# Kernel optimization log

Hardware: AMD Instinct MI355X
Metric: run time of the kernel (lower is better)

Reference implementation:

```python
import jax, jax.numpy as jnp
import numpy as np

N = 50000      # nodes
E = 800000     # edges (avg degree 16)
F_IN = 256
HID = 256
N_CLASSES = 128


def setup_inputs() -> dict:
    key = jax.random.key(0)
    ks = jax.random.split(key, 12)
    x = jax.random.normal(ks[0], (N, F_IN), dtype=jnp.float32)
    src = jax.random.randint(ks[1], (E,), 0, N)
    dst = jax.random.randint(ks[2], (E,), 0, N)
    inp = {"x": x, "src": src, "dst": dst}
    dims = [(F_IN, HID), (HID, HID), (HID, N_CLASSES)]
    for l, (din, dout) in enumerate(dims):
        s = 1.0 / np.sqrt(din)
        inp[f"W_self_{l}"] = jax.random.uniform(ks[3 + 3 * l], (dout, din), jnp.float32, -s, s)
        inp[f"W_neigh_{l}"] = jax.random.uniform(ks[4 + 3 * l], (dout, din), jnp.float32, -s, s)
        inp[f"b_{l}"] = jnp.zeros((dout,), jnp.float32)
    return inp


def _mean_agg(h, src, dst, n):
    # mean over in-neighbors: gather src features, segment-sum into dst, divide by in-degree
    s = jax.ops.segment_sum(h[src], dst, num_segments=n)          # [N, F]
    deg = jax.ops.segment_sum(jnp.ones((src.shape[0],), h.dtype), dst, num_segments=n)
    return s / jnp.maximum(deg, 1.0)[:, None]


def reference(x, W_self_0, W_neigh_0, b_0, W_self_1, W_neigh_1, b_1,
              W_self_2, W_neigh_2, b_2, src, dst):
    # DGL SAGEConv('mean'): out = fc_self(h_dst) + fc_neigh(mean_neigh(h)) + bias
    layers = [(W_self_0, W_neigh_0, b_0),
              (W_self_1, W_neigh_1, b_1),
              (W_self_2, W_neigh_2, b_2)]
    n = x.shape[0]
    h = x
    for l, (Ws, Wn, b) in enumerate(layers):
        agg = _mean_agg(h, src, dst, n)
        h = h @ Ws.T + agg @ Wn.T + b
        if l != len(layers) - 1:
            h = jax.nn.relu(h)  # dropout p=0 -> identity
    return h
```

## Files before the change

### kernel.cpp

```cpp
#include <hip/hip_runtime.h>
#include <stdint.h>

#define NNODES 50000
#define NEDGES 800000
#define NB_SCAN ((NNODES + 255) / 256)
#define NB_CVTX 12500
#define NB_CVTW 384
#define NB_HIST 3125

typedef _Float16 f16;
typedef _Float16 f16x4 __attribute__((ext_vector_type(4)));
typedef _Float16 f16x8 __attribute__((ext_vector_type(8)));
typedef float f32x4 __attribute__((ext_vector_type(4)));
typedef float f32x8 __attribute__((ext_vector_type(8)));

static inline size_t align_up(size_t x, size_t a){ return (x + a - 1) & ~(a - 1); }

__device__ __forceinline__ void gll16(const void* g, void* l){
  __builtin_amdgcn_global_load_lds((const __attribute__((address_space(1))) uint32_t*)(g),
                                   (__attribute__((address_space(3))) uint32_t*)(l), 16, 0, 0);
}

__device__ __forceinline__ f16x8 ld8(const f16* p){ return *reinterpret_cast<const f16x8*>(p); }

__global__ void __launch_bounds__(256) k_pre(const float* __restrict__ x, f16* __restrict__ xh,
                       const float* __restrict__ a0, const float* __restrict__ a1,
                       const float* __restrict__ a2, const float* __restrict__ a3,
                       const float* __restrict__ a4, const float* __restrict__ a5,
                       f16* __restrict__ o0, f16* __restrict__ o1, f16* __restrict__ o2,
                       f16* __restrict__ o3, f16* __restrict__ o4, f16* __restrict__ o5,
                       const int* __restrict__ dst, int* __restrict__ deg){
  int b = blockIdx.x;
  int tid = threadIdx.x;
  if (b < NB_CVTX){
    int i = b * 256 + tid;
    float4 v = *reinterpret_cast<const float4*>(&x[(size_t)i * 4]);
    f16x4 o = { (f16)v.x, (f16)v.y, (f16)v.z, (f16)v.w };
    *reinterpret_cast<f16x4*>(&xh[(size_t)i * 4]) = o;
  } else if (b < NB_CVTX + NB_CVTW){
    int bb = b - NB_CVTX;
    int seg = bb >> 6;
    const float* in; f16* out; int n;
    switch (seg){
      case 0: in = a0; out = o0; n = 65536; break;
      case 1: in = a1; out = o1; n = 65536; break;
      case 2: in = a2; out = o2; n = 65536; break;
      case 3: in = a3; out = o3; n = 65536; break;
      case 4: in = a4; out = o4; n = 32768; break;
      default: in = a5; out = o5; n = 32768; break;
    }
    int i = ((bb & 63) * 256 + tid) * 4;
    if (i < n){
      float4 v = *reinterpret_cast<const float4*>(&in[i]);
      f16x4 o = { (f16)v.x, (f16)v.y, (f16)v.z, (f16)v.w };
      *reinterpret_cast<f16x4*>(&out[i]) = o;
    }
  } else {
    int i = (b - NB_CVTX - NB_CVTW) * 256 + tid;
    if (i < NEDGES) atomicAdd(&deg[dst[i]], 1);
  }
}

__global__ void __launch_bounds__(256) k_scan1(const int* __restrict__ deg,
                        int* __restrict__ row_ptr, int* __restrict__ bsum, int n){
  __shared__ int s[256];
  int tid = threadIdx.x;
  int i = blockIdx.x * 256 + tid;
  int v = (i < n) ? deg[i] : 0;
  s[tid] = v;
  __syncthreads();
  #pragma unroll
  for (int off = 1; off < 256; off <<= 1){
    int t = (tid >= off) ? s[tid - off] : 0;
    __syncthreads();
    s[tid] += t;
    __syncthreads();
  }
  if (i < n) row_ptr[i] = s[tid] - v;
  if (tid == 255) bsum[blockIdx.x] = s[255];
}

__global__ void __launch_bounds__(256) k_scan2(const int* __restrict__ bsum,
                        int* __restrict__ boff, int* __restrict__ row_ptr, int nb, int n){
  __shared__ int s[256];
  int tid = threadIdx.x;
  int v = (tid < nb) ? bsum[tid] : 0;
  s[tid] = v;
  __syncthreads();
  #pragma unroll
  for (int off = 1; off < 256; off <<= 1){
    int t = (tid >= off) ? s[tid - off] : 0;
    __syncthreads();
    s[tid] += t;
    __syncthreads();
  }
  if (tid < nb) boff[tid] = s[tid] - v;
  if (tid == 255) row_ptr[n] = s[255];
}

__global__ void __launch_bounds__(256) k_scan3(int* __restrict__ row_ptr,
                        const int* __restrict__ boff, int* __restrict__ cursor, int n){
  int i = blockIdx.x * 256 + threadIdx.x;
  if (i < n){
    int v = row_ptr[i] + boff[blockIdx.x];
    row_ptr[i] = v;
    cursor[i] = v;
  }
}

__global__ void k_fill(const int* __restrict__ src, const int* __restrict__ dst,
                       int* __restrict__ cursor, int* __restrict__ csr, int e){
  int i = blockIdx.x * blockDim.x + threadIdx.x;
  if (i < e){
    int p = atomicAdd(&cursor[dst[i]], 1);
    csr[p] = src[i];
  }
}

__global__ void __launch_bounds__(256) k_mm(const f16* __restrict__ A,
                                            const f16* __restrict__ Bw,
                                            f16* __restrict__ C, int M, int N){
  __shared__ __align__(16) char sA[16384];
  __shared__ __align__(16) char sB[16384];
  int nwg = gridDim.x;
  int q = nwg >> 3, r = nwg & 7;
  int xcd = blockIdx.x & 7, seq = blockIdx.x >> 3;
  int t = (xcd < r) ? xcd * (q + 1) + seq : r * (q + 1) + (xcd - r) * q + seq;
  int nbn = N >> 7;
  int mi = t / nbn, ni = t - mi * nbn;
  int m0 = mi * 128, n0 = ni * 128;

  int tid = threadIdx.x;
  int lane = tid & 63, wid = tid >> 6;
  int wm = (wid & 1) * 64, wn = (wid >> 1) * 64;

  f32x4 acc[4][4];
  #pragma unroll
  for (int m = 0; m < 4; ++m)
    #pragma unroll
    for (int n = 0; n < 4; ++n)
      acc[m][n] = (f32x4){0.f, 0.f, 0.f, 0.f};

  const int srow = tid >> 3;
  const int scolx = ((tid & 7) << 4) ^ ((srow & 7) << 4);
  const char* Ab = (const char*)A;
  const char* Bb = (const char*)Bw;

  for (int kt = 0; kt < 4; ++kt){
    int kbyte = kt * 128;
    if (kt) __syncthreads();
    #pragma unroll
    for (int qq = 0; qq < 4; ++qq){
      int row = qq * 32 + srow;
      int ga = m0 + row; if (ga >= M) ga = M - 1;
      int gb = n0 + row;
      gll16(Ab + (size_t)ga * 512 + kbyte + scolx, sA + qq * 4096 + wid * 1024);
      gll16(Bb + (size_t)gb * 512 + kbyte + scolx, sB + qq * 4096 + wid * 1024);
    }
    __syncthreads();
    #pragma unroll
    for (int kk = 0; kk < 2; ++kk){
      int cb = kk * 64 + ((lane >> 4) << 4);
      f16x8 af[4], bfr[4];
      #pragma unroll
      for (int m = 0; m < 4; ++m){
        int rr = wm + m * 16 + (lane & 15);
        af[m] = *reinterpret_cast<const f16x8*>(sA + rr * 128 + (cb ^ ((rr & 7) << 4)));
      }
      #pragma unroll
      for (int n = 0; n < 4; ++n){
        int rr = wn + n * 16 + (lane & 15);
        bfr[n] = *reinterpret_cast<const f16x8*>(sB + rr * 128 + (cb ^ ((rr & 7) << 4)));
      }
      #pragma unroll
      for (int m = 0; m < 4; ++m)
        #pragma unroll
        for (int n = 0; n < 4; ++n)
          acc[m][n] = __builtin_amdgcn_mfma_f32_16x16x32_f16(af[m], bfr[n], acc[m][n], 0, 0, 0);
    }
  }

  int cl = lane & 15, rq = lane >> 4;
  #pragma unroll
  for (int n = 0; n < 4; ++n){
    int gc = n0 + wn + n * 16 + cl;
    #pragma unroll
    for (int m = 0; m < 4; ++m){
      int gr0 = m0 + wm + m * 16 + rq * 4;
      #pragma unroll
      for (int j = 0; j < 4; ++j){
        int gr = gr0 + j;
        if (gr < M) C[(size_t)gr * N + gc] = (f16)acc[m][n][j];
      }
    }
  }
}

__global__ void __launch_bounds__(256) k_comb(const f16* __restrict__ sp,
                        const int* __restrict__ row_ptr,
                        const int* __restrict__ csr,
                        const float* __restrict__ bias,
                        f16* __restrict__ h){
  int wid = threadIdx.x >> 6, lane = threadIdx.x & 63;
  int node = blockIdx.x * 4 + wid;
  if (node >= NNODES) return;
  int s = row_ptr[node], e = row_ptr[node + 1];
  int hh = lane >> 5, fl = lane & 31;
  const f16* pbase = sp + 256 + (size_t)fl * 8;
  f32x8 accA = {0,0,0,0,0,0,0,0}, accB = {0,0,0,0,0,0,0,0};
  int p = s + hh;
  while (p + 2 < e){
    int j0 = csr[p], j1 = csr[p + 2];
    f16x8 v0 = ld8(pbase + (size_t)j0 * 512);
    f16x8 v1 = ld8(pbase + (size_t)j1 * 512);
    #pragma unroll
    for (int c = 0; c < 8; ++c){ accA[c] += (float)v0[c]; accB[c] += (float)v1[c]; }
    p += 4;
  }
  if (p < e){
    int j = csr[p];
    f16x8 v = ld8(pbase + (size_t)j * 512);
    #pragma unroll
    for (int c = 0; c < 8; ++c) accA[c] += (float)v[c];
  }
  #pragma unroll
  for (int c = 0; c < 8; ++c){
    float t = accA[c] + accB[c];
    accA[c] = t + __shfl_xor(t, 32);
  }
  int d = e - s;
  float inv = (d > 0) ? 1.f / (float)d : 0.f;
  if (lane < 32){
    f16x8 sv = ld8(&sp[(size_t)node * 512 + fl * 8]);
    float4 ba = *reinterpret_cast<const float4*>(&bias[fl * 8]);
    float4 bb = *reinterpret_cast<const float4*>(&bias[fl * 8 + 4]);
    float bv[8] = {ba.x, ba.y, ba.z, ba.w, bb.x, bb.y, bb.z, bb.w};
    f16x8 o;
    #pragma unroll
    for (int c = 0; c < 8; ++c){
      float x = (float)sv[c] + bv[c] + accA[c] * inv;
      o[c] = (f16)fmaxf(x, 0.f);
    }
    *reinterpret_cast<f16x8*>(&h[(size_t)node * 256 + fl * 8]) = o;
  }
}

__global__ void __launch_bounds__(256) k_comb2(const f16* __restrict__ sp,
                        const int* __restrict__ row_ptr,
                        const int* __restrict__ csr,
                        const float* __restrict__ bias,
                        float* __restrict__ out){
  int wid = threadIdx.x >> 6, lane = threadIdx.x & 63;
  int node = blockIdx.x * 4 + wid;
  if (node >= NNODES) return;
  int s = row_ptr[node], e = row_ptr[node + 1];
  int hh = lane >> 4, fl = lane & 15;
  const f16* pbase = sp + 128 + (size_t)fl * 8;
  f32x8 accA = {0,0,0,0,0,0,0,0}, accB = {0,0,0,0,0,0,0,0};
  int p = s + hh;
  while (p + 4 < e){
    int j0 = csr[p], j1 = csr[p + 4];
    f16x8 v0 = ld8(pbase + (size_t)j0 * 256);
    f16x8 v1 = ld8(pbase + (size_t)j1 * 256);
    #pragma unroll
    for (int c = 0; c < 8; ++c){ accA[c] += (float)v0[c]; accB[c] += (float)v1[c]; }
    p += 8;
  }
  if (p < e){
    int j = csr[p];
    f16x8 v = ld8(pbase + (size_t)j * 256);
    #pragma unroll
    for (int c = 0; c < 8; ++c) accA[c] += (float)v[c];
  }
  #pragma unroll
  for (int c = 0; c < 8; ++c){
    float t = accA[c] + accB[c];
    t += __shfl_xor(t, 16);
    accA[c] = t + __shfl_xor(t, 32);
  }
  int d = e - s;
  float inv = (d > 0) ? 1.f / (float)d : 0.f;
  if (lane < 16){
    f16x8 sv = ld8(&sp[(size_t)node * 256 + fl * 8]);
    float4 ba = *reinterpret_cast<const float4*>(&bias[fl * 8]);
    float4 bb = *reinterpret_cast<const float4*>(&bias[fl * 8 + 4]);
    float4 o1, o2;
    o1.x = (float)sv[0] + ba.x + accA[0] * inv;
    o1.y = (float)sv[1] + ba.y + accA[1] * inv;
    o1.z = (float)sv[2] + ba.z + accA[2] * inv;
    o1.w = (float)sv[3] + ba.w + accA[3] * inv;
    o2.x = (float)sv[4] + bb.x + accA[4] * inv;
    o2.y = (float)sv[5] + bb.y + accA[5] * inv;
    o2.z = (float)sv[6] + bb.z + accA[6] * inv;
    o2.w = (float)sv[7] + bb.w + accA[7] * inv;
    *reinterpret_cast<float4*>(&out[(size_t)node * 128 + fl * 8]) = o1;
    *reinterpret_cast<float4*>(&out[(size_t)node * 128 + fl * 8 + 4]) = o2;
  }
}

extern "C" void kernel_launch(void* const* d_in, const int* in_sizes, int n_in,
                              void* d_out, int out_size, void* d_ws, size_t ws_size,
                              hipStream_t stream){
  const float* x   = (const float*)d_in[0];
  const int*   src = (const int*)d_in[1];
  const int*   dst = (const int*)d_in[2];
  const float* Ws0 = (const float*)d_in[3];
  const float* Wn0 = (const float*)d_in[4];
  const float* b0  = (const float*)d_in[5];
  const float* Ws1 = (const float*)d_in[6];
  const float* Wn1 = (const float*)d_in[7];
  const float* b1  = (const float*)d_in[8];
  const float* Ws2 = (const float*)d_in[9];
  const float* Wn2 = (const float*)d_in[10];
  const float* b2  = (const float*)d_in[11];
  float* out = (float*)d_out;

  char* ws = (char*)d_ws;
  size_t off = 0;
  int* deg     = (int*)(ws + off); off = align_up(off + (size_t)NNODES * 4, 256);
  int* row_ptr = (int*)(ws + off); off = align_up(off + (size_t)(NNODES + 1) * 4, 256);
  int* cursor  = (int*)(ws + off); off = align_up(off + (size_t)NNODES * 4, 256);
  int* csr     = (int*)(ws + off); off = align_up(off + (size_t)NEDGES * 4, 256);
  int* bsum    = (int*)(ws + off); off = align_up(off + (size_t)256 * 4, 256);
  int* boff    = (int*)(ws + off); off = align_up(off + (size_t)256 * 4, 256);
  f16* xh   = (f16*)(ws + off); off = align_up(off + (size_t)NNODES * 256 * 2, 256);
  f16* hA   = (f16*)(ws + off); off = align_up(off + (size_t)NNODES * 256 * 2, 256);
  f16* sp   = (f16*)(ws + off); off = align_up(off + (size_t)NNODES * 512 * 2, 256);
  f16* w16  = (f16*)(ws + off); off = align_up(off + (size_t)327680 * 2, 256);
  f16* Ws0h = w16;              f16* Wn0h = w16 + 65536;
  f16* Ws1h = w16 + 131072;     f16* Wn1h = w16 + 196608;
  f16* Ws2h = w16 + 262144;     f16* Wn2h = w16 + 294912;
  f16* hB = xh;
  (void)ws_size; (void)in_sizes; (void)n_in; (void)out_size;

  hipMemsetAsync(deg, 0, (size_t)NNODES * 4, stream);
  k_pre<<<NB_CVTX + NB_CVTW + NB_HIST, 256, 0, stream>>>(
      x, xh, Ws0, Wn0, Ws1, Wn1, Ws2, Wn2,
      Ws0h, Wn0h, Ws1h, Wn1h, Ws2h, Wn2h, dst, deg);
  k_scan1<<<NB_SCAN, 256, 0, stream>>>(deg, row_ptr, bsum, NNODES);
  k_scan2<<<1, 256, 0, stream>>>(bsum, boff, row_ptr, NB_SCAN, NNODES);
  k_scan3<<<NB_SCAN, 256, 0, stream>>>(row_ptr, boff, cursor, NNODES);
  k_fill<<<(NEDGES + 255) / 256, 256, 0, stream>>>(src, dst, cursor, csr, NEDGES);

  int gm = (NNODES + 127) / 128;
  int gc = (NNODES + 3) / 4;
  k_mm<<<gm * 4, 256, 0, stream>>>(xh, Ws0h, sp, NNODES, 512);
  k_comb<<<gc, 256, 0, stream>>>(sp, row_ptr, csr, b0, hA);
  k_mm<<<gm * 4, 256, 0, stream>>>(hA, Ws1h, sp, NNODES, 512);
  k_comb<<<gc, 256, 0, stream>>>(sp, row_ptr, csr, b1, hB);
  k_mm<<<gm * 2, 256, 0, stream>>>(hB, Ws2h, sp, NNODES, 256);
  k_comb2<<<gc, 256, 0, stream>>>(sp, row_ptr, csr, b2, out);
}
```

Before: 335.1 us.

## Double-buffer GEMM LDS tiles and coalesce output stores via LDS staging

The GEMM kernel now prefetches the next K tile into a second LDS buffer while computing on the current one, replacing load-then-compute with a two-stage pipeline. The epilogue stages each wave's 16x64 output block through padded LDS and writes 16-byte vector rows instead of scattered scalar half stores. LDS usage doubles to 64 KB, which may reduce occupancy, and the short K loop limits how much overlap is available.

After: 327.6 us. -2.2%, faster.

```diff
diff --git a/kernel.cpp b/kernel.cpp
--- a/kernel.cpp
+++ b/kernel.cpp
@@ -120,8 +120,7 @@
 __global__ void __launch_bounds__(256) k_mm(const f16* __restrict__ A,
                                             const f16* __restrict__ Bw,
                                             f16* __restrict__ C, int M, int N){
-  __shared__ __align__(16) char sA[16384];
-  __shared__ __align__(16) char sB[16384];
+  __shared__ __align__(16) char sm[65536];
   int nwg = gridDim.x;
   int q = nwg >> 3, r = nwg & 7;
   int xcd = blockIdx.x & 7, seq = blockIdx.x >> 3;
@@ -146,9 +145,10 @@
   const char* Ab = (const char*)A;
   const char* Bb = (const char*)Bw;
 
-  for (int kt = 0; kt < 4; ++kt){
+  auto STAGE = [&](int kt, int buf){
     int kbyte = kt * 128;
-    if (kt) __syncthreads();
+    char* sA = sm + buf * 16384;
+    char* sB = sm + 32768 + buf * 16384;
     #pragma unroll
     for (int qq = 0; qq < 4; ++qq){
       int row = qq * 32 + srow;
@@ -157,7 +157,15 @@
       gll16(Ab + (size_t)ga * 512 + kbyte + scolx, sA + qq * 4096 + wid * 1024);
       gll16(Bb + (size_t)gb * 512 + kbyte + scolx, sB + qq * 4096 + wid * 1024);
     }
-    __syncthreads();
+  };
+
+  STAGE(0, 0);
+  __syncthreads();
+  for (int kt = 0; kt < 4; ++kt){
+    int buf = kt & 1;
+    if (kt < 3) STAGE(kt + 1, buf ^ 1);
+    const char* sA = sm + buf * 16384;
+    const char* sB = sm + 32768 + buf * 16384;
     #pragma unroll
     for (int kk = 0; kk < 2; ++kk){
       int cb = kk * 64 + ((lane >> 4) << 4);
@@ -178,20 +186,26 @@
         for (int n = 0; n < 4; ++n)
           acc[m][n] = __builtin_amdgcn_mfma_f32_16x16x32_f16(af[m], bfr[n], acc[m][n], 0, 0, 0);
     }
-  }
-
+    __syncthreads();
+  }
+
+  f16* ep = (f16*)(sm + wid * 2304);
   int cl = lane & 15, rq = lane >> 4;
   #pragma unroll
-  for (int n = 0; n < 4; ++n){
-    int gc = n0 + wn + n * 16 + cl;
-    #pragma unroll
-    for (int m = 0; m < 4; ++m){
-      int gr0 = m0 + wm + m * 16 + rq * 4;
+  for (int m = 0; m < 4; ++m){
+    #pragma unroll
+    for (int n = 0; n < 4; ++n)
       #pragma unroll
-      for (int j = 0; j < 4; ++j){
-        int gr = gr0 + j;
-        if (gr < M) C[(size_t)gr * N + gc] = (f16)acc[m][n][j];
-      }
+      for (int j = 0; j < 4; ++j)
+        ep[(rq * 4 + j) * 68 + n * 16 + cl] = (f16)acc[m][n][j];
+    #pragma unroll
+    for (int pass = 0; pass < 2; ++pass){
+      int row = (lane >> 3) + pass * 8;
+      int col8 = (lane & 7) * 8;
+      f16x8 v = *reinterpret_cast<const f16x8*>(&ep[row * 68 + col8]);
+      int gr = m0 + wm + m * 16 + row;
+      if (gr < M)
+        *reinterpret_cast<f16x8*>(&C[(size_t)gr * N + n0 + wn + col8]) = v;
     }
   }
 }
```
